# Optimization experiments

Measured on AMD Instinct MI355X. Metric: run time of the kernel, lower is better.

The kernel has to match this reference:

```python
import jax, jax.numpy as jnp
import numpy as np

GRID = 5
N = GRID * GRID          # 25 control points
OUT_H, OUT_W = 256, 192
BATCH = 64


def _make_consts():
    # Pixel grid in [-0.9, 0.9]
    gx, gy = np.meshgrid(np.linspace(-0.9, 0.9, OUT_W),
                         np.linspace(-0.9, 0.9, OUT_H))
    # Control points (note torch code: P_Y, P_X = meshgrid(coords, coords))
    coords = np.linspace(-0.9, 0.9, GRID)
    P_Y, P_X = np.meshgrid(coords, coords)
    Px = P_X.reshape(N)
    Py = P_Y.reshape(N)
    # TPS kernel matrix and L inverse (float32, matching torch default dtype)
    d2 = (Px[:, None] - Px[None, :]) ** 2 + (Py[:, None] - Py[None, :]) ** 2
    d2[d2 == 0] = 1.0
    K = d2 * np.log(d2)
    P = np.stack([np.ones(N), Px, Py], axis=1)          # [N,3]
    L = np.block([[K, P], [P.T, np.zeros((3, 3))]]).astype(np.float32)
    Li = np.linalg.inv(L)
    return (gx.astype(np.float32), gy.astype(np.float32),
            Px.astype(np.float32), Py.astype(np.float32),
            Li.astype(np.float32))


def setup_inputs() -> dict:
    key = jax.random.key(0)
    theta = jax.random.normal(key, (BATCH, 2 * N), dtype=jnp.float32)
    gx, gy, Px, Py, Li = _make_consts()
    return {
        "theta": theta,
        "gx": jnp.asarray(gx), "gy": jnp.asarray(gy),
        "Px": jnp.asarray(Px), "Py": jnp.asarray(Py),
        "Li": jnp.asarray(Li),
    }


def reference(theta, gx, gy, Px, Py, Li):
    # Displaced control points Q = theta + base control points  [B,N]
    Qx = theta[:, :N] + Px
    Qy = theta[:, N:] + Py
    # TPS coefficients: nonlinear weights W [B,N], affine A [B,3]
    Wx = jnp.einsum('nm,bm->bn', Li[:N, :N], Qx)
    Wy = jnp.einsum('nm,bm->bn', Li[:N, :N], Qy)
    Ax = jnp.einsum('km,bm->bk', Li[N:, :N], Qx)
    Ay = jnp.einsum('km,bm->bk', Li[N:, :N], Qy)
    # RBF kernel U(r) = r^2 log(r^2) per pixel per control point  [H,W,N]
    d2 = (gx[..., None] - Px) ** 2 + (gy[..., None] - Py) ** 2
    d2 = jnp.where(d2 == 0, 1.0, d2)   # torch sets d2==0 -> 1 so U=0 there
    U = d2 * jnp.log(d2)
    # Warped coordinates  [B,H,W]
    Xp = (Ax[:, 0, None, None]
          + Ax[:, 1, None, None] * gx
          + Ax[:, 2, None, None] * gy
          + jnp.einsum('hwn,bn->bhw', U, Wx))
    Yp = (Ay[:, 0, None, None]
          + Ay[:, 1, None, None] * gx
          + Ay[:, 2, None, None] * gy
          + jnp.einsum('hwn,bn->bhw', U, Wy))
    return jnp.stack([Xp, Yp], axis=-1)   # [B,H,W,2]
```

## Files before the change

### kernel.cpp

```cpp
#include <hip/hip_runtime.h>


#define HW_PIX (256 * 192)
#define NB 64

__global__ __launch_bounds__(64) void tps_coef_kernel(
    const float* __restrict__ theta, const float* __restrict__ Px,
    const float* __restrict__ Py, const float* __restrict__ Li,
    float* __restrict__ cf)
{
    const int b = blockIdx.x;
    const int t = threadIdx.x;
    if (t >= 56) return;
    bool is_y; int row;
    if (t < 3)       { is_y = false; row = 25 + t; }
    else if (t < 6)  { is_y = true;  row = 25 + (t - 3); }
    else if (t < 31) { is_y = false; row = t - 6; }
    else             { is_y = true;  row = t - 31; }
    const float* P  = is_y ? Py : Px;
    const float* th = theta + b * 50 + (is_y ? 25 : 0);
    const float* L  = Li + row * 28;
    float s = 0.f;
    #pragma unroll
    for (int m = 0; m < 25; ++m)
        s = fmaf(L[m], th[m] + P[m], s);
    cf[(b << 6) + t] = s;
}

__global__ __launch_bounds__(256) void tps_main_kernel(
    const float* __restrict__ gx, const float* __restrict__ gy,
    const float* __restrict__ Px, const float* __restrict__ Py,
    const float* __restrict__ cf, float* __restrict__ out)
{
    const int lane = threadIdx.x & 63;
    const int wave = __builtin_amdgcn_readfirstlane(threadIdx.x >> 6);
    const int p = blockIdx.x * 64 + lane;

    const float x = gx[p];
    const float y = gy[p];

    float dx2[5], dy2[5];
    #pragma unroll
    for (int i = 0; i < 5; ++i) {
        float dx = x - Px[5 * i];
        float dy = y - Py[i];
        dx2[i] = dx * dx;
        dy2[i] = dy * dy;
    }

    float u[25];
    #pragma unroll
    for (int n = 0; n < 25; ++n) {
        float d2 = dx2[n / 5] + dy2[n % 5];
        u[n] = d2 * __logf(fmaxf(d2, 1e-30f));
    }

    float2* out2 = (float2*)out;
    const int b0 = (blockIdx.y * 4 + wave) * 4;
    #pragma unroll
    for (int bi = 0; bi < 4; ++bi) {
        const int b = b0 + bi;
        const float* c = cf + (b << 6);
        float X = fmaf(c[1], x, c[0]);
        X = fmaf(c[2], y, X);
        float Y = fmaf(c[4], x, c[3]);
        Y = fmaf(c[5], y, Y);
        #pragma unroll
        for (int n = 0; n < 25; ++n) {
            X = fmaf(u[n], c[6 + n], X);
            Y = fmaf(u[n], c[31 + n], Y);
        }
        out2[b * HW_PIX + p] = make_float2(X, Y);
    }
}

extern "C" void kernel_launch(void* const* d_in, const int* in_sizes, int n_in,
                              void* d_out, int out_size, void* d_ws, size_t ws_size,
                              hipStream_t stream) {
    const float* theta = (const float*)d_in[0];
    const float* gx    = (const float*)d_in[1];
    const float* gy    = (const float*)d_in[2];
    const float* Px    = (const float*)d_in[3];
    const float* Py    = (const float*)d_in[4];
    const float* Li    = (const float*)d_in[5];
    float* out = (float*)d_out;
    float* cf  = (float*)d_ws;

    tps_coef_kernel<<<dim3(NB), dim3(64), 0, stream>>>(theta, Px, Py, Li, cf);
    tps_main_kernel<<<dim3(HW_PIX / 64, 4), dim3(256), 0, stream>>>(gx, gy, Px, Py, cf, out);
}
```

Measured before the change: 24.14 us.

## Fuse coefficient solve into main kernel via per-pixel Li-transposed weights

Removes the separate coefficient kernel by reassociating the math: each pixel computes v = Li^T-projected basis (affine rows plus U-weighted Li rows), then the output per batch is a dot product of v with theta plus a precomputed Px/Py term. This removes one kernel launch and the workspace round trip. In exchange each pixel does a 25x25 FMA block redundantly (~700 extra FMAs per pixel), amortized over 16 batches per thread, and the grid is reshaped to 256 pixels per block with 16 batches per thread. Floating-point summation order changes.

```diff
diff --git a/kernel.cpp b/kernel.cpp
--- a/kernel.cpp
+++ b/kernel.cpp
@@ -3,39 +3,16 @@
 
 #define HW_PIX (256 * 192)
 #define NB 64
+#define BSPLIT 4
+#define NBW (NB / BSPLIT)
 
-__global__ __launch_bounds__(64) void tps_coef_kernel(
-    const float* __restrict__ theta, const float* __restrict__ Px,
+__global__ __launch_bounds__(256) void tps_fused_kernel(
+    const float* __restrict__ theta, const float* __restrict__ gx,
+    const float* __restrict__ gy, const float* __restrict__ Px,
     const float* __restrict__ Py, const float* __restrict__ Li,
-    float* __restrict__ cf)
+    float* __restrict__ out)
 {
-    const int b = blockIdx.x;
-    const int t = threadIdx.x;
-    if (t >= 56) return;
-    bool is_y; int row;
-    if (t < 3)       { is_y = false; row = 25 + t; }
-    else if (t < 6)  { is_y = true;  row = 25 + (t - 3); }
-    else if (t < 31) { is_y = false; row = t - 6; }
-    else             { is_y = true;  row = t - 31; }
-    const float* P  = is_y ? Py : Px;
-    const float* th = theta + b * 50 + (is_y ? 25 : 0);
-    const float* L  = Li + row * 28;
-    float s = 0.f;
-    #pragma unroll
-    for (int m = 0; m < 25; ++m)
-        s = fmaf(L[m], th[m] + P[m], s);
-    cf[(b << 6) + t] = s;
-}
-
-__global__ __launch_bounds__(256) void tps_main_kernel(
-    const float* __restrict__ gx, const float* __restrict__ gy,
-    const float* __restrict__ Px, const float* __restrict__ Py,
-    const float* __restrict__ cf, float* __restrict__ out)
-{
-    const int lane = threadIdx.x & 63;
-    const int wave = __builtin_amdgcn_readfirstlane(threadIdx.x >> 6);
-    const int p = blockIdx.x * 64 + lane;
-
+    const int p = blockIdx.x * 256 + threadIdx.x;
     const float x = gx[p];
     const float y = gy[p];
 
@@ -47,7 +24,6 @@
         dx2[i] = dx * dx;
         dy2[i] = dy * dy;
     }
-
     float u[25];
     #pragma unroll
     for (int n = 0; n < 25; ++n) {
@@ -55,20 +31,42 @@
         u[n] = d2 * __logf(fmaxf(d2, 1e-30f));
     }
 
+    float v[25];
+    {
+        const float* L25 = Li + 25 * 28;
+        const float* L26 = Li + 26 * 28;
+        const float* L27 = Li + 27 * 28;
+        #pragma unroll
+        for (int m = 0; m < 25; ++m)
+            v[m] = fmaf(L27[m], y, fmaf(L26[m], x, L25[m]));
+    }
+    #pragma unroll
+    for (int n = 0; n < 25; ++n) {
+        const float un = u[n];
+        const float* Lr = Li + n * 28;
+        #pragma unroll
+        for (int m = 0; m < 25; ++m)
+            v[m] = fmaf(Lr[m], un, v[m]);
+    }
+
+    float cx = 0.f, cy = 0.f;
+    #pragma unroll
+    for (int m = 0; m < 25; ++m) {
+        cx = fmaf(Px[m], v[m], cx);
+        cy = fmaf(Py[m], v[m], cy);
+    }
+
     float2* out2 = (float2*)out;
-    const int b0 = (blockIdx.y * 4 + wave) * 4;
+    const int b0 = blockIdx.y * NBW;
     #pragma unroll
-    for (int bi = 0; bi < 4; ++bi) {
+    for (int bi = 0; bi < NBW; ++bi) {
         const int b = b0 + bi;
-        const float* c = cf + (b << 6);
-        float X = fmaf(c[1], x, c[0]);
-        X = fmaf(c[2], y, X);
-        float Y = fmaf(c[4], x, c[3]);
-        Y = fmaf(c[5], y, Y);
+        const float* tb = theta + b * 50;
+        float X = cx, Y = cy;
         #pragma unroll
-        for (int n = 0; n < 25; ++n) {
-            X = fmaf(u[n], c[6 + n], X);
-            Y = fmaf(u[n], c[31 + n], Y);
+        for (int m = 0; m < 25; ++m) {
+            X = fmaf(tb[m],      v[m], X);
+            Y = fmaf(tb[25 + m], v[m], Y);
         }
         out2[b * HW_PIX + p] = make_float2(X, Y);
     }
@@ -84,8 +82,7 @@
     const float* Py    = (const float*)d_in[4];
     const float* Li    = (const float*)d_in[5];
     float* out = (float*)d_out;
-    float* cf  = (float*)d_ws;
 
-    tps_coef_kernel<<<dim3(NB), dim3(64), 0, stream>>>(theta, Px, Py, Li, cf);
-    tps_main_kernel<<<dim3(HW_PIX / 64, 4), dim3(256), 0, stream>>>(gx, gy, Px, Py, cf, out);
+    tps_fused_kernel<<<dim3(HW_PIX / 256, BSPLIT), dim3(256), 0, stream>>>(
+        theta, gx, gy, Px, Py, Li, out);
 }
```

Result: faster. 20.56 us (-14.8%).
